# Optimization experiments

Hardware: AMD Instinct MI355X
Metric: run time of the kernel (lower is better)

The kernel has to match this reference:

```python
import jax, jax.numpy as jnp
import numpy as np

D_MODEL, D_CTX, D_HEAD = 1024, 768, 16

def setup_inputs() -> dict:
    key = jax.random.key(0)
    ks = jax.random.split(key, 10)
    B, M, N = 8, 4096, 4096
    s = lambda d: 1.0 / np.sqrt(d)
    return {
        "x": jax.random.normal(ks[0], (B, M, D_MODEL), dtype=jnp.float32),
        "context": jax.random.normal(ks[1], (B, N, D_CTX), dtype=jnp.float32),
        "Wq": jax.random.uniform(ks[2], (D_MODEL, D_HEAD), jnp.float32, -s(D_MODEL), s(D_MODEL)),
        "bq": jax.random.uniform(ks[3], (D_HEAD,), jnp.float32, -s(D_MODEL), s(D_MODEL)),
        "Wk": jax.random.uniform(ks[4], (D_CTX, D_HEAD), jnp.float32, -s(D_CTX), s(D_CTX)),
        "bk": jax.random.uniform(ks[5], (D_HEAD,), jnp.float32, -s(D_CTX), s(D_CTX)),
        "Wv": jax.random.uniform(ks[6], (D_CTX, D_HEAD), jnp.float32, -s(D_CTX), s(D_CTX)),
        "bv": jax.random.uniform(ks[7], (D_HEAD,), jnp.float32, -s(D_CTX), s(D_CTX)),
        "Wo": jax.random.uniform(ks[8], (D_HEAD, D_MODEL), jnp.float32, -s(D_HEAD), s(D_HEAD)),
        "bo": jax.random.uniform(ks[9], (D_MODEL,), jnp.float32, -s(D_HEAD), s(D_HEAD)),
    }

def _kernel(t):
    # ELU+1 feature map (non-negative)
    return jax.nn.elu(t) + 1.0

def reference(x, context, Wq, bq, Wk, bk, Wv, bv, Wo, bo):
    Q = _kernel(x @ Wq + bq)            # (B, M, d_head)
    K = _kernel(context @ Wk + bk)      # (B, N, d_head)
    V = context @ Wv + bv               # (B, N, d_head)
    KtV = jnp.einsum('bnd,bne->bde', K, V)   # (B, d_head, d_head)
    num = jnp.einsum('bmd,bde->bme', Q, KtV) # (B, M, d_head)
    K_sum = K.sum(axis=1)                    # (B, d_head)
    denom = jnp.einsum('bmd,bd->bm', Q, K_sum)[..., None] + 1e-6
    out = num / denom                        # (B, M, d_head)
    return out @ Wo + bo                     # (B, M, d_model)
```

## Files before the change

kernel.cpp:

```cpp
#include <hip/hip_runtime.h>
#include <math.h>

#define B_   8
#define M_   4096
#define N_   4096
#define DM   1024
#define DC   768
#define DH   16
#define CHUNKS 64
#define XS   136
#define NCHQ (DM/128)
#define NCHK (DC/128)

typedef float v4f __attribute__((ext_vector_type(4)));
typedef __attribute__((ext_vector_type(8))) short short8v;
typedef __attribute__((ext_vector_type(4))) float f32x4;
typedef __attribute__((ext_vector_type(4))) int int4v;

__device__ __forceinline__ float elu1(float t) {
    return t > 0.0f ? t + 1.0f : expf(t);
}
__device__ __forceinline__ float4 ld4(const float* p) { return *reinterpret_cast<const float4*>(p); }
__device__ __forceinline__ void  st4(float* p, float4 v) { *reinterpret_cast<float4*>(p) = v; }
__device__ __forceinline__ void  st4nt(float* p, float4 v) {
    v4f w; w.x = v.x; w.y = v.y; w.z = v.z; w.w = v.w;
    __builtin_nontemporal_store(w, reinterpret_cast<v4f*>(p));
}
__device__ __forceinline__ void fma4(float4& a, float s, float4 w) {
    a.x = fmaf(s, w.x, a.x); a.y = fmaf(s, w.y, a.y);
    a.z = fmaf(s, w.z, a.z); a.w = fmaf(s, w.w, a.w);
}
__device__ __forceinline__ short f2bf(float f) {
    unsigned u = __float_as_uint(f);
    unsigned r = 0x7FFFu + ((u >> 16) & 1u);
    return (short)((u + r) >> 16);
}
__device__ __forceinline__ unsigned cvtpk(float a, float b) {
    unsigned r;
    asm("v_cvt_pk_bf16_f32 %0, %1, %2" : "=v"(r) : "v"(a), "v"(b));
    return r;
}

__global__ __launch_bounds__(256) void prep(
    const float* __restrict__ Wq, const float* __restrict__ Wk,
    const float* __restrict__ Wv,
    short* __restrict__ fq, short* __restrict__ fk, short* __restrict__ fv)
{
    const int id = blockIdx.x * 256 + threadIdx.x;
    if (id >= 80 * 64) return;
    const int l  = id & 63;
    const int kt = id >> 6;
    const float* W; short* dst; int ktl;
    if (kt < 32)      { W = Wq; dst = fq; ktl = kt; }
    else if (kt < 56) { W = Wk; dst = fk; ktl = kt - 32; }
    else              { W = Wv; dst = fv; ktl = kt - 56; }
    const int k0 = ktl * 32 + (l >> 4) * 8;
    const int d  = l & 15;
    short* o = dst + ((size_t)ktl * 64 + l) * 8;
    #pragma unroll
    for (int j = 0; j < 8; ++j)
        o[j] = f2bf(W[(size_t)(k0 + j) * DH + d]);
}

__global__ __launch_bounds__(256) void fused1(
    const float* __restrict__ ctx, const float* __restrict__ x,
    const short* __restrict__ fq, const short* __restrict__ fk,
    const short* __restrict__ fv,
    const float* __restrict__ bq, const float* __restrict__ bk,
    const float* __restrict__ bv,
    float* __restrict__ part, float* __restrict__ q_ws)
{
    __shared__ union {
        short xt[64 * XS];
        struct { float k[64][17]; float v[64][17]; } kv;
    } sh;

    const int t  = threadIdx.x;
    const int l  = t & 63;
    const int w  = t >> 6;
    const int g4 = l >> 4;
    const int lr = l & 15;

    float4 A[8];

#define SLOADX(src, LD, ch) { \
    _Pragma("unroll") for (int i = 0; i < 4; ++i) { \
        const int fi = 2*t + i*512; \
        const int rr = fi >> 5; const int cc = fi & 31; \
        const float* p = (src) + (row0 + rr)*(LD) + (ch)*128 + cc*4; \
        A[2*i] = ld4(p); A[2*i+1] = ld4(p + 4); } }
#define SWRITEX() { \
    _Pragma("unroll") for (int i = 0; i < 4; ++i) { \
        const int fi = 2*t + i*512; \
        const int rr = fi >> 5; const int cc = fi & 31; \
        int4v wv4; \
        wv4.x = (int)cvtpk(A[2*i].x,   A[2*i].y); \
        wv4.y = (int)cvtpk(A[2*i].z,   A[2*i].w); \
        wv4.z = (int)cvtpk(A[2*i+1].x, A[2*i+1].y); \
        wv4.w = (int)cvtpk(A[2*i+1].z, A[2*i+1].w); \
        *reinterpret_cast<int4v*>(reinterpret_cast<char*>(&sh.xt[0]) + rr*272 + cc*8) = wv4; } }

    if (blockIdx.x < B_*N_/64) {
        const size_t row0 = (size_t)blockIdx.x * 64;
        f32x4 accK = {0,0,0,0}, accV = {0,0,0,0};

        SLOADX(ctx, DC, 0);
        for (int ch = 0; ch < NCHK; ++ch) {
            SWRITEX();
            __syncthreads();
            if (ch + 1 < NCHK) SLOADX(ctx, DC, ch + 1);
            #pragma unroll
            for (int kt = 0; kt < 4; ++kt) {
                const short8v a = *reinterpret_cast<const short8v*>(
                    &sh.xt[(w*16 + lr)*XS + kt*32 + g4*8]);
                const int ktg = ch*4 + kt;
                const short8v bkf = *reinterpret_cast<const short8v*>(fk + ((size_t)ktg*64 + l)*8);
                const short8v bvf = *reinterpret_cast<const short8v*>(fv + ((size_t)ktg*64 + l)*8);
                accK = __builtin_amdgcn_mfma_f32_16x16x32_bf16(a, bkf, accK, 0, 0, 0);
                accV = __builtin_amdgcn_mfma_f32_16x16x32_bf16(a, bvf, accV, 0, 0, 0);
            }
            __syncthreads();
        }

        const float bkv = bk[lr], bvv = bv[lr];
        #pragma unroll
        for (int j = 0; j < 4; ++j) {
            const int n = w*16 + g4*4 + j;
            sh.kv.k[n][lr] = elu1(accK[j] + bkv);
            sh.kv.v[n][lr] = accV[j] + bvv;
        }
        __syncthreads();

        const int d = t >> 4, e = t & 15;
        float acc = 0.f;
        #pragma unroll 16
        for (int n = 0; n < 64; ++n) acc += sh.kv.k[n][d] * sh.kv.v[n][e];
        float* p = part + (size_t)blockIdx.x * 272;
        p[t] = acc;
        if (t < DH) {
            float ss = 0.f;
            #pragma unroll 16
            for (int n = 0; n < 64; ++n) ss += sh.kv.k[n][t];
            p[256 + t] = ss;
        }
    } else {
        const size_t row0 = (size_t)(blockIdx.x - B_*N_/64) * 64;
        f32x4 accQ = {0,0,0,0};

        SLOADX(x, DM, 0);
        for (int ch = 0; ch < NCHQ; ++ch) {
            SWRITEX();
            __syncthreads();
            if (ch + 1 < NCHQ) SLOADX(x, DM, ch + 1);
            #pragma unroll
            for (int kt = 0; kt < 4; ++kt) {
                const short8v a = *reinterpret_cast<const short8v*>(
                    &sh.xt[(w*16 + lr)*XS + kt*32 + g4*8]);
                const int ktg = ch*4 + kt;
                const short8v bqf = *reinterpret_cast<const short8v*>(fq + ((size_t)ktg*64 + l)*8);
                accQ = __builtin_amdgcn_mfma_f32_16x16x32_bf16(a, bqf, accQ, 0, 0, 0);
            }
            __syncthreads();
        }

        const float bqv = bq[lr];
        #pragma unroll
        for (int j = 0; j < 4; ++j) {
            const int n = w*16 + g4*4 + j;
            q_ws[(row0 + n)*DH + lr] = elu1(accQ[j] + bqv);
        }
    }
#undef SLOADX
#undef SWRITEX
}

__global__ __launch_bounds__(320) void reduce2(
    const float* __restrict__ part, float* __restrict__ comb)
{
    const int b = blockIdx.x;
    const int t = threadIdx.x;
    if (t < 272) {
        float s = 0.f;
        #pragma unroll
        for (int ch = 0; ch < CHUNKS; ++ch)
            s += part[((size_t)b*CHUNKS + ch) * 272 + t];
        comb[(size_t)b*272 + t] = s;
    }
}

__global__ __launch_bounds__(256) void oproj(
    const float* __restrict__ q_ws, const float* __restrict__ comb,
    const float* __restrict__ Wo, const float* __restrict__ bo,
    float* __restrict__ out)
{
    __shared__ float ql[16 * DH];
    __shared__ float ol[16 * DH];
    __shared__ float kts[272];

    const int t = threadIdx.x;
    const size_t row0 = (size_t)blockIdx.x * 16;
    const int b = blockIdx.x >> 8;

    float4 wreg[16];
    #pragma unroll
    for (int e = 0; e < 16; ++e) wreg[e] = ld4(Wo + (size_t)e*DM + t*4);
    const float4 bov = ld4(bo + t*4);

    if (t < 64) st4(&ql[t*4], ld4(q_ws + row0*DH + t*4));
    else if (t < 132) st4(&kts[(t-64)*4], ld4(comb + (size_t)b*272 + (t-64)*4));
    __syncthreads();

    if (t < 64) {
        const float* qrow = &ql[(t >> 2) * DH];
        const int jj = (t & 3) * 4;
        float den = 1e-6f;
        float4 num = make_float4(0,0,0,0);
        #pragma unroll
        for (int d4 = 0; d4 < 4; ++d4) {
            const float4 q4  = ld4(&qrow[d4*4]);
            const float4 ks4 = ld4(&kts[256 + d4*4]);
            den += q4.x*ks4.x + q4.y*ks4.y + q4.z*ks4.z + q4.w*ks4.w;
            fma4(num, q4.x, ld4(&kts[(d4*4+0)*DH + jj]));
            fma4(num, q4.y, ld4(&kts[(d4*4+1)*DH + jj]));
            fma4(num, q4.z, ld4(&kts[(d4*4+2)*DH + jj]));
            fma4(num, q4.w, ld4(&kts[(d4*4+3)*DH + jj]));
        }
        const float inv = 1.0f / den;
        float4 o4; o4.x = num.x*inv; o4.y = num.y*inv; o4.z = num.z*inv; o4.w = num.w*inv;
        st4(&ol[(t >> 2)*DH + jj], o4);
    }
    __syncthreads();

    #pragma unroll
    for (int r = 0; r < 16; ++r) {
        float4 a = bov;
        #pragma unroll
        for (int eo = 0; eo < 4; ++eo) {
            const float4 o4 = ld4(&ol[r*DH + eo*4]);
            fma4(a, o4.x, wreg[eo*4+0]); fma4(a, o4.y, wreg[eo*4+1]);
            fma4(a, o4.z, wreg[eo*4+2]); fma4(a, o4.w, wreg[eo*4+3]);
        }
        st4nt(out + (row0 + r)*DM + t*4, a);
    }
}

extern "C" void kernel_launch(void* const* d_in, const int* in_sizes, int n_in,
                              void* d_out, int out_size, void* d_ws, size_t ws_size,
                              hipStream_t stream) {
    const float* x    = (const float*)d_in[0];
    const float* ctx  = (const float*)d_in[1];
    const float* Wq   = (const float*)d_in[2];
    const float* bq   = (const float*)d_in[3];
    const float* Wk   = (const float*)d_in[4];
    const float* bk   = (const float*)d_in[5];
    const float* Wv   = (const float*)d_in[6];
    const float* bv   = (const float*)d_in[7];
    const float* Wo   = (const float*)d_in[8];
    const float* bo   = (const float*)d_in[9];
    float* out = (float*)d_out;

    float* ws = (float*)d_ws;
    float* part = ws;
    float* comb = part + (size_t)512*272;
    float* q_ws = comb + (size_t)B_*272;
    short* fq = (short*)(q_ws + (size_t)B_*M_*DH);
    short* fk = fq + (size_t)32*64*8;
    short* fv = fk + (size_t)24*64*8;

    prep<<<dim3(20), dim3(256), 0, stream>>>(Wq, Wk, Wv, fq, fk, fv);
    fused1<<<dim3(B_*N_/64 + B_*M_/64), dim3(256), 0, stream>>>(
        ctx, x, fq, fk, fv, bq, bk, bv, part, q_ws);
    reduce2<<<dim3(B_), dim3(320), 0, stream>>>(part, comb);
    oproj<<<dim3(B_*M_/16), dim3(256), 0, stream>>>(q_ws, comb, Wo, bo, out);
}
```

Measured before the change: 82.38 us.

## Load MFMA A-fragments directly from global with register prefetch ring, drop LDS staging

The projection GEMM in fused1 no longer stages x/context tiles through shared memory with barriers. Each lane now loads its own 8-float A-fragment straight from global memory and converts it to bf16 in registers, using an 8-deep register ring to prefetch ahead. This removes the LDS round-trip and the __syncthreads per chunk. In exchange, each lane's global loads become strided 32-byte pieces per row instead of coalesced row segments, and register pressure rises.

```diff
diff --git a/kernel.cpp b/kernel.cpp
--- a/kernel.cpp
+++ b/kernel.cpp
@@ -8,9 +8,7 @@
 #define DC   768
 #define DH   16
 #define CHUNKS 64
-#define XS   136
-#define NCHQ (DM/128)
-#define NCHK (DC/128)
+#define PD   8
 
 typedef float v4f __attribute__((ext_vector_type(4)));
 typedef __attribute__((ext_vector_type(8))) short short8v;
@@ -39,6 +37,15 @@
     unsigned r;
     asm("v_cvt_pk_bf16_f32 %0, %1, %2" : "=v"(r) : "v"(a), "v"(b));
     return r;
+}
+__device__ __forceinline__ short8v mk_frag(const float4& a, const float4& b) {
+    int4v iv;
+    iv.x = (int)cvtpk(a.x, a.y);
+    iv.y = (int)cvtpk(a.z, a.w);
+    iv.z = (int)cvtpk(b.x, b.y);
+    iv.w = (int)cvtpk(b.z, b.w);
+    union { int4v i; short8v s; } u; u.i = iv;
+    return u.s;
 }
 
 __global__ __launch_bounds__(256) void prep(
@@ -70,10 +77,8 @@
     const float* __restrict__ bv,
     float* __restrict__ part, float* __restrict__ q_ws)
 {
-    __shared__ union {
-        short xt[64 * XS];
-        struct { float k[64][17]; float v[64][17]; } kv;
-    } sh;
+    __shared__ float sk[64][DH+1];
+    __shared__ float sv[64][DH+1];
 
     const int t  = threadIdx.x;
     const int l  = t & 63;
@@ -81,86 +86,73 @@
     const int g4 = l >> 4;
     const int lr = l & 15;
 
-    float4 A[8];
-
-#define SLOADX(src, LD, ch) { \
-    _Pragma("unroll") for (int i = 0; i < 4; ++i) { \
-        const int fi = 2*t + i*512; \
-        const int rr = fi >> 5; const int cc = fi & 31; \
-        const float* p = (src) + (row0 + rr)*(LD) + (ch)*128 + cc*4; \
-        A[2*i] = ld4(p); A[2*i+1] = ld4(p + 4); } }
-#define SWRITEX() { \
-    _Pragma("unroll") for (int i = 0; i < 4; ++i) { \
-        const int fi = 2*t + i*512; \
-        const int rr = fi >> 5; const int cc = fi & 31; \
-        int4v wv4; \
-        wv4.x = (int)cvtpk(A[2*i].x,   A[2*i].y); \
-        wv4.y = (int)cvtpk(A[2*i].z,   A[2*i].w); \
-        wv4.z = (int)cvtpk(A[2*i+1].x, A[2*i+1].y); \
-        wv4.w = (int)cvtpk(A[2*i+1].z, A[2*i+1].w); \
-        *reinterpret_cast<int4v*>(reinterpret_cast<char*>(&sh.xt[0]) + rr*272 + cc*8) = wv4; } }
+    float4 pa[PD], pb[PD];
 
     if (blockIdx.x < B_*N_/64) {
         const size_t row0 = (size_t)blockIdx.x * 64;
+        const float* src = ctx + (row0 + w*16 + lr) * DC + g4*8;
         f32x4 accK = {0,0,0,0}, accV = {0,0,0,0};
 
-        SLOADX(ctx, DC, 0);
-        for (int ch = 0; ch < NCHK; ++ch) {
-            SWRITEX();
-            __syncthreads();
-            if (ch + 1 < NCHK) SLOADX(ctx, DC, ch + 1);
-            #pragma unroll
-            for (int kt = 0; kt < 4; ++kt) {
-                const short8v a = *reinterpret_cast<const short8v*>(
-                    &sh.xt[(w*16 + lr)*XS + kt*32 + g4*8]);
-                const int ktg = ch*4 + kt;
-                const short8v bkf = *reinterpret_cast<const short8v*>(fk + ((size_t)ktg*64 + l)*8);
-                const short8v bvf = *reinterpret_cast<const short8v*>(fv + ((size_t)ktg*64 + l)*8);
-                accK = __builtin_amdgcn_mfma_f32_16x16x32_bf16(a, bkf, accK, 0, 0, 0);
-                accV = __builtin_amdgcn_mfma_f32_16x16x32_bf16(a, bvf, accV, 0, 0, 0);
+        #pragma unroll
+        for (int i = 0; i < PD; ++i) {
+            pa[i] = ld4(src + i*32);
+            pb[i] = ld4(src + i*32 + 4);
+        }
+        #pragma unroll
+        for (int kt = 0; kt < 24; ++kt) {
+            const int st = kt & (PD-1);
+            const short8v a = mk_frag(pa[st], pb[st]);
+            if (kt + PD < 24) {
+                pa[st] = ld4(src + (kt+PD)*32);
+                pb[st] = ld4(src + (kt+PD)*32 + 4);
             }
-            __syncthreads();
+            const short8v bkf = *reinterpret_cast<const short8v*>(fk + ((size_t)kt*64 + l)*8);
+            const short8v bvf = *reinterpret_cast<const short8v*>(fv + ((size_t)kt*64 + l)*8);
+            accK = __builtin_amdgcn_mfma_f32_16x16x32_bf16(a, bkf, accK, 0, 0, 0);
+            accV = __builtin_amdgcn_mfma_f32_16x16x32_bf16(a, bvf, accV, 0, 0, 0);
         }
 
         const float bkv = bk[lr], bvv = bv[lr];
         #pragma unroll
         for (int j = 0; j < 4; ++j) {
             const int n = w*16 + g4*4 + j;
-            sh.kv.k[n][lr] = elu1(accK[j] + bkv);
-            sh.kv.v[n][lr] = accV[j] + bvv;
+            sk[n][lr] = elu1(accK[j] + bkv);
+            sv[n][lr] = accV[j] + bvv;
         }
         __syncthreads();
 
         const int d = t >> 4, e = t & 15;
         float acc = 0.f;
         #pragma unroll 16
-        for (int n = 0; n < 64; ++n) acc += sh.kv.k[n][d] * sh.kv.v[n][e];
+        for (int n = 0; n < 64; ++n) acc += sk[n][d] * sv[n][e];
         float* p = part + (size_t)blockIdx.x * 272;
         p[t] = acc;
         if (t < DH) {
             float ss = 0.f;
             #pragma unroll 16
-            for (int n = 0; n < 64; ++n) ss += sh.kv.k[n][t];
+            for (int n = 0; n < 64; ++n) ss += sk[n][t];
             p[256 + t] = ss;
         }
     } else {
         const size_t row0 = (size_t)(blockIdx.x - B_*N_/64) * 64;
+        const float* src = x + (row0 + w*16 + lr) * DM + g4*8;
         f32x4 accQ = {0,0,0,0};
 
-        SLOADX(x, DM, 0);
-        for (int ch = 0; ch < NCHQ; ++ch) {
-            SWRITEX();
-            __syncthreads();
-            if (ch + 1 < NCHQ) SLOADX(x, DM, ch + 1);
-            #pragma unroll
-            for (int kt = 0; kt < 4; ++kt) {
-                const short8v a = *reinterpret_cast<const short8v*>(
-                    &sh.xt[(w*16 + lr)*XS + kt*32 + g4*8]);
-                const int ktg = ch*4 + kt;
-                const short8v bqf = *reinterpret_cast<const short8v*>(fq + ((size_t)ktg*64 + l)*8);
-                accQ = __builtin_amdgcn_mfma_f32_16x16x32_bf16(a, bqf, accQ, 0, 0, 0);
+        #pragma unroll
+        for (int i = 0; i < PD; ++i) {
+            pa[i] = ld4(src + i*32);
+            pb[i] = ld4(src + i*32 + 4);
+        }
+        #pragma unroll
+        for (int kt = 0; kt < 32; ++kt) {
+            const int st = kt & (PD-1);
+            const short8v a = mk_frag(pa[st], pb[st]);
+            if (kt + PD < 32) {
+                pa[st] = ld4(src + (kt+PD)*32);
+                pb[st] = ld4(src + (kt+PD)*32 + 4);
             }
-            __syncthreads();
+            const short8v bqf = *reinterpret_cast<const short8v*>(fq + ((size_t)kt*64 + l)*8);
+            accQ = __builtin_amdgcn_mfma_f32_16x16x32_bf16(a, bqf, accQ, 0, 0, 0);
         }
 
         const float bqv = bq[lr];
@@ -170,8 +162,6 @@
             q_ws[(row0 + n)*DH + lr] = elu1(accQ[j] + bqv);
         }
     }
-#undef SLOADX
-#undef SWRITEX
 }
 
 __global__ __launch_bounds__(320) void reduce2(
```

New measurement: 79.75 us. 3.2% less time.
